# Optimization experiments

Measured on AMD Instinct MI355X. Metric: run time of the kernel, lower is better.

Reference implementation:

```python
import jax, jax.numpy as jnp
import numpy as np

PI = float(np.pi)

def _quantize_angle(theta):
    deg = theta * (180.0 / PI)
    deg = jnp.where(deg < 0, deg + 180.0, deg)
    q = jnp.round(deg / 45.0) * 45.0
    # 180 is treated the same as 0 in the original branch (theta==0 or theta==180)
    return jnp.where(q == 180.0, 0.0, q)

def setup_inputs() -> dict:
    key = jax.random.key(0)
    k1, k2 = jax.random.split(key)
    H, W = 4096, 4096
    img = jax.random.uniform(k1, (1, 1, H, W), dtype=jnp.float32)
    theta = jax.random.normal(k2, (1, 1, H, W), dtype=jnp.float32)  # radians
    return {"img": img, "theta": theta}

def reference(img, theta):
    q = _quantize_angle(theta)

    # value of neighbor at (x+dx, y+dy); borders are masked out afterwards so
    # roll wrap-around never affects the result (interior pixels only).
    def nbr(dx, dy):
        return jnp.roll(img, shift=(-dx, -dy), axis=(2, 3))

    def local_max(dx, dy):
        return (img >= nbr(dx, dy)) & (img >= nbr(-dx, -dy))

    m0 = local_max(0, 1)     # theta == 0 / 180: compare (x, y+-1)
    m45 = local_max(1, 1)    # theta == 45:      compare (x+-1, y+-1)
    m90 = local_max(1, 0)    # theta == 90:      compare (x+-1, y)
    m135 = local_max(1, -1)  # theta == 135:     compare (x+1,y-1),(x-1,y+1)

    mask = jnp.where(q == 0.0, m0,
           jnp.where(q == 45.0, m45,
           jnp.where(q == 90.0, m90, m135)))

    H, W = img.shape[2], img.shape[3]
    interior = jnp.zeros((H, W), dtype=bool).at[1:-1, 1:-1].set(True)
    return jnp.where(mask & interior, img, jnp.zeros_like(img))
```

## Files before the change

### kernel.cpp

```cpp
#include <hip/hip_runtime.h>
#include <math.h>

#define IMG_H 4096
#define IMG_W 4096
#define RPT 4

__device__ __forceinline__ float nms_px(float t, bool interior,
                                        float uL, float uC, float uR,
                                        float cL, float cC, float cR,
                                        float dL, float dC, float dR) {
    float deg = t * 57.29577951308232f;
    deg = (deg < 0.0f) ? deg + 180.0f : deg;
    float q = rintf(deg / 45.0f) * 45.0f;
    const bool is0  = (q == 0.0f) || (q == 180.0f);
    const bool is45 = (q == 45.0f);
    const bool is90 = (q == 90.0f);
    const float a = is0 ? cR : (is45 ? dR : (is90 ? dC : dL));
    const float b = is0 ? cL : (is45 ? uL : (is90 ? uC : uR));
    return ((cC >= a) && (cC >= b) && interior) ? cC : 0.0f;
}

__global__ __launch_bounds__(256) void nms_kernel(const float* __restrict__ img,
                                                  const float* __restrict__ theta,
                                                  float* __restrict__ out) {
    const int tid = blockIdx.x * blockDim.x + threadIdx.x;
    const int g  = tid >> 10;
    const int y4 = (tid & 1023) << 2;
    const int x0 = g * RPT;

    const int yl = (y4 > 0)         ? y4 - 1 : 0;
    const int yr = (y4 + 4 < IMG_W) ? y4 + 4 : IMG_W - 1;

    const bool col0_int = (y4 > 0);
    const bool col3_int = (y4 + 4 < IMG_W);

    float4 u, c, d;
    float ul, ur, cl, cr, dl, dr;

    {
        const int xu0 = (x0 > 0) ? x0 - 1 : 0;
        const float* __restrict__ pr = img + (size_t)xu0 * IMG_W;
        u = *(const float4*)(pr + y4); ul = pr[yl]; ur = pr[yr];
    }
    {
        const float* __restrict__ pr = img + (size_t)x0 * IMG_W;
        c = *(const float4*)(pr + y4); cl = pr[yl]; cr = pr[yr];
    }

    #pragma unroll
    for (int i = 0; i < RPT; ++i) {
        const int x  = x0 + i;
        const int xd = (x < IMG_H - 1) ? x + 1 : IMG_H - 1;
        {
            const float* __restrict__ pr = img + (size_t)xd * IMG_W;
            d = *(const float4*)(pr + y4); dl = pr[yl]; dr = pr[yr];
        }

        const size_t base = (size_t)x * IMG_W + y4;
        const float4 th = *(const float4*)(theta + base);

        const bool row_int = (x > 0) && (x < IMG_H - 1);

        float4 o;
        o.x = nms_px(th.x, row_int && col0_int, ul,  u.x, u.y,  cl,  c.x, c.y,  dl,  d.x, d.y);
        o.y = nms_px(th.y, row_int,             u.x, u.y, u.z,  c.x, c.y, c.z,  d.x, d.y, d.z);
        o.z = nms_px(th.z, row_int,             u.y, u.z, u.w,  c.y, c.z, c.w,  d.y, d.z, d.w);
        o.w = nms_px(th.w, row_int && col3_int, u.z, u.w, ur,   c.z, c.w, cr,   d.z, d.w, dr);

        *(float4*)(out + base) = o;

        u = c; ul = cl; ur = cr;
        c = d; cl = dl; cr = dr;
    }
}

extern "C" void kernel_launch(void* const* d_in, const int* in_sizes, int n_in,
                              void* d_out, int out_size, void* d_ws, size_t ws_size,
                              hipStream_t stream) {
    const float* img   = (const float*)d_in[0];
    const float* theta = (const float*)d_in[1];
    float* out = (float*)d_out;

    const int total_threads = (IMG_H / RPT) * (IMG_W / 4);
    const int block = 256;
    const int grid = total_threads / block;
    nms_kernel<<<grid, block, 0, stream>>>(img, theta, out);
}
```

Measured before the change: 170.4 us.

## Use wave shuffles for horizontal halos, prefetch next row, nontemporal theta/out

Each wave now covers 256 contiguous columns and fetches the left and right neighbours from adjacent lanes with shuffles, so only the two edge lanes issue scalar halo loads. The next image row and theta row are software-prefetched one iteration ahead, rows per thread go from 4 to 8, and theta loads and output stores use nontemporal hints. The aim is fewer redundant scalar loads and better latency hiding in a bandwidth-bound stencil. The trade-offs are extra shuffle instructions, higher register pressure, and fewer threads overall.

```diff
diff --git a/kernel.cpp b/kernel.cpp
--- a/kernel.cpp
+++ b/kernel.cpp
@@ -3,7 +3,10 @@
 
 #define IMG_H 4096
 #define IMG_W 4096
-#define RPT 4
+#define RPT 8
+#define WPR (IMG_W / 256)
+
+typedef float floatx4 __attribute__((ext_vector_type(4)));
 
 __device__ __forceinline__ float nms_px(float t, bool interior,
                                         float uL, float uC, float uR,
@@ -23,54 +26,72 @@
 __global__ __launch_bounds__(256) void nms_kernel(const float* __restrict__ img,
                                                   const float* __restrict__ theta,
                                                   float* __restrict__ out) {
-    const int tid = blockIdx.x * blockDim.x + threadIdx.x;
-    const int g  = tid >> 10;
-    const int y4 = (tid & 1023) << 2;
+    const int gtid = blockIdx.x * 256 + threadIdx.x;
+    const int wave = gtid >> 6;
+    const int lane = gtid & 63;
+    const int g  = wave / WPR;
+    const int wc = (wave % WPR) << 8;
+    const int y4 = wc + (lane << 2);
     const int x0 = g * RPT;
 
-    const int yl = (y4 > 0)         ? y4 - 1 : 0;
-    const int yr = (y4 + 4 < IMG_W) ? y4 + 4 : IMG_W - 1;
+    const bool is_l = (lane == 0);
+    const bool is_r = (lane == 63);
+    const bool edge_lane = is_l || is_r;
+    const int ye = is_l ? (wc > 0 ? wc - 1 : 0)
+                        : (wc + 256 < IMG_W ? wc + 256 : IMG_W - 1);
 
-    const bool col0_int = (y4 > 0);
-    const bool col3_int = (y4 + 4 < IMG_W);
+    const bool c0_int = (y4 > 0);
+    const bool c3_int = (y4 + 4 < IMG_W);
 
-    float4 u, c, d;
-    float ul, ur, cl, cr, dl, dr;
+    auto load_row = [&](int x, floatx4& v, float& e) {
+        const float* __restrict__ pr = img + (size_t)x * IMG_W;
+        v = *(const floatx4*)(pr + y4);
+        e = 0.0f;
+        if (edge_lane) e = pr[ye];
+    };
 
-    {
-        const int xu0 = (x0 > 0) ? x0 - 1 : 0;
-        const float* __restrict__ pr = img + (size_t)xu0 * IMG_W;
-        u = *(const float4*)(pr + y4); ul = pr[yl]; ur = pr[yr];
-    }
-    {
-        const float* __restrict__ pr = img + (size_t)x0 * IMG_W;
-        c = *(const float4*)(pr + y4); cl = pr[yl]; cr = pr[yr];
-    }
+    floatx4 u, c, d, d_nxt;
+    float ue, ce, de, de_nxt;
+    floatx4 th, th_nxt;
+
+    load_row((x0 > 0) ? x0 - 1 : 0, u, ue);
+    load_row(x0, c, ce);
+    load_row((x0 + 1 < IMG_H) ? x0 + 1 : IMG_H - 1, d, de);
+    th = *(const floatx4*)(theta + (size_t)x0 * IMG_W + y4);
 
     #pragma unroll
     for (int i = 0; i < RPT; ++i) {
-        const int x  = x0 + i;
-        const int xd = (x < IMG_H - 1) ? x + 1 : IMG_H - 1;
-        {
-            const float* __restrict__ pr = img + (size_t)xd * IMG_W;
-            d = *(const float4*)(pr + y4); dl = pr[yl]; dr = pr[yr];
+        const int x = x0 + i;
+
+        if (i < RPT - 1) {
+            const int xn = (x + 2 < IMG_H) ? x + 2 : IMG_H - 1;
+            load_row(xn, d_nxt, de_nxt);
+            const float* tp = theta + (size_t)(x + 1) * IMG_W + y4;
+            th_nxt = __builtin_nontemporal_load((const floatx4*)tp);
         }
 
-        const size_t base = (size_t)x * IMG_W + y4;
-        const float4 th = *(const float4*)(theta + base);
+        float uLs = __shfl_up(u.w, 1, 64), uRs = __shfl_down(u.x, 1, 64);
+        float cLs = __shfl_up(c.w, 1, 64), cRs = __shfl_down(c.x, 1, 64);
+        float dLs = __shfl_up(d.w, 1, 64), dRs = __shfl_down(d.x, 1, 64);
+        const float uL = is_l ? ue : uLs, uR = is_r ? ue : uRs;
+        const float cL = is_l ? ce : cLs, cR = is_r ? ce : cRs;
+        const float dL = is_l ? de : dLs, dR = is_r ? de : dRs;
 
         const bool row_int = (x > 0) && (x < IMG_H - 1);
 
-        float4 o;
-        o.x = nms_px(th.x, row_int && col0_int, ul,  u.x, u.y,  cl,  c.x, c.y,  dl,  d.x, d.y);
-        o.y = nms_px(th.y, row_int,             u.x, u.y, u.z,  c.x, c.y, c.z,  d.x, d.y, d.z);
-        o.z = nms_px(th.z, row_int,             u.y, u.z, u.w,  c.y, c.z, c.w,  d.y, d.z, d.w);
-        o.w = nms_px(th.w, row_int && col3_int, u.z, u.w, ur,   c.z, c.w, cr,   d.z, d.w, dr);
+        floatx4 o;
+        o.x = nms_px(th.x, row_int && c0_int, uL,  u.x, u.y,  cL,  c.x, c.y,  dL,  d.x, d.y);
+        o.y = nms_px(th.y, row_int,           u.x, u.y, u.z,  c.x, c.y, c.z,  d.x, d.y, d.z);
+        o.z = nms_px(th.z, row_int,           u.y, u.z, u.w,  c.y, c.z, c.w,  d.y, d.z, d.w);
+        o.w = nms_px(th.w, row_int && c3_int, u.z, u.w, uR,   c.z, c.w, cR,   d.z, d.w, dR);
 
-        *(float4*)(out + base) = o;
+        floatx4* po = (floatx4*)(out + (size_t)x * IMG_W + y4);
+        __builtin_nontemporal_store(o, po);
 
-        u = c; ul = cl; ur = cr;
-        c = d; cl = dl; cr = dr;
+        u = c; ue = ce;
+        c = d; ce = de;
+        d = d_nxt; de = de_nxt;
+        th = th_nxt;
     }
 }
 
@@ -81,7 +102,7 @@
     const float* theta = (const float*)d_in[1];
     float* out = (float*)d_out;
 
-    const int total_threads = (IMG_H / RPT) * (IMG_W / 4);
+    const int total_threads = (IMG_H / RPT) * WPR * 64;
     const int block = 256;
     const int grid = total_threads / block;
     nms_kernel<<<grid, block, 0, stream>>>(img, theta, out);
```

Measured after the change: 171.8 us. About the same (+0.8%).
